# Performance work log

Measured on AMD Instinct MI355X. Metric: run time of the kernel, lower is better.

## Reference

```python
import jax, jax.numpy as jnp
import numpy as np

SIGMA_D = 0.2
SIGMA_A = 15.0
FACTOR_A = 180.0 / (SIGMA_A * np.pi)
HIDDEN = 256


def sinusoidal_embedding(x, d_model):
    # GeoTransformer-style: interleaved sin/cos pairs along last dim.
    div_term = jnp.exp(jnp.arange(0, d_model, 2, dtype=x.dtype) * (-np.log(10000.0) / d_model))  # (d/2,)
    omegas = x[..., None] * div_term  # (..., d/2)
    emb = jnp.stack([jnp.sin(omegas), jnp.cos(omegas)], axis=-1)  # (..., d/2, 2)
    return emb.reshape(*x.shape, d_model)


def _indices(points, anchor_points):
    # pairwise sq dist: |p|^2 + |a|^2 - 2 p.a, clamped at 0
    sq = (jnp.sum(points ** 2, -1)[:, :, None]
          + jnp.sum(anchor_points ** 2, -1)[:, None, :]
          - 2.0 * jnp.einsum('bnd,bkd->bnk', points, anchor_points))
    dist_map = jnp.sqrt(jnp.maximum(sq, 0.0))  # (B,N,K)
    d_indices = dist_map / SIGMA_D
    ref_vectors = points[:, :, None, :] - anchor_points[:, None, :, :]  # (B,N,K,3)
    # gather with indices [1,2,...,K-1,0] == roll by -1 along K
    anc_vectors = jnp.roll(ref_vectors, shift=-1, axis=2)
    sin_values = jnp.linalg.norm(jnp.cross(ref_vectors, anc_vectors, axis=-1), axis=-1)
    cos_values = jnp.sum(ref_vectors * anc_vectors, axis=-1)
    angles = jnp.arctan2(sin_values, cos_values)
    a_indices = angles * FACTOR_A
    return d_indices, a_indices


def setup_inputs() -> dict:
    key = jax.random.key(0)
    ks = jax.random.split(key, 5)
    B, N, K, H = 1, 4096, 64, HIDDEN
    return {
        'points': jax.random.normal(ks[0], (B, N, 3), jnp.float32),
        'anchor_points': jax.random.normal(ks[1], (B, K, 3), jnp.float32),
        'cor_score': jax.random.uniform(ks[2], (K,), jnp.float32),
        'Wa': jax.random.normal(ks[3], (H, H), jnp.float32) * (1.0 / np.sqrt(H)),
        'ba': jnp.zeros((H,), jnp.float32),
        'Wd': jax.random.normal(ks[4], (H, H), jnp.float32) * (1.0 / np.sqrt(H)),
        'bd': jnp.zeros((H,), jnp.float32),
    }


def reference(points, anchor_points, cor_score, Wa, ba, Wd, bd):
    d_idx, a_idx = _indices(points, anchor_points)  # computed under no_grad in torch
    d_idx = jax.lax.stop_gradient(d_idx)
    a_idx = jax.lax.stop_gradient(a_idx)
    a_emb = sinusoidal_embedding(a_idx, HIDDEN)          # (B,N,K,H)
    a_emb = jnp.einsum('bnkh,oh->bnko', a_emb, Wa) + ba
    d_emb = sinusoidal_embedding(d_idx, HIDDEN)
    d_emb = jnp.einsum('bnkh,oh->bnko', d_emb, Wd) + bd
    # reduction_a == 'max'
    d_emb = jnp.max(d_emb, axis=2)
    a_emb = jnp.max(a_emb, axis=2)
    return d_emb + a_emb  # (B,N,H)
```

## Files before the change

### kernel.cpp

```cpp
#include <hip/hip_runtime.h>
#include <hip/hip_bf16.h>
#include <math.h>


typedef __attribute__((ext_vector_type(8))) short short8;
typedef __attribute__((ext_vector_type(16))) float f32x16;
typedef __attribute__((ext_vector_type(4))) unsigned int uint4v;
typedef __attribute__((ext_vector_type(4))) float float4v;
typedef __attribute__((ext_vector_type(4))) unsigned short ushort4v;

#define HH 256
#define KK 112
#define P_PTS 8
#define NPTS 4096

__device__ __forceinline__ unsigned short f2bf(float f) {
    union { float f; unsigned int u; } v; v.f = f;
    unsigned int r = v.u + 0x7fffu + ((v.u >> 16) & 1u);
    return (unsigned short)(r >> 16);
}

__device__ __forceinline__ unsigned int pack_sc(float s, float c) {
    union { __hip_bfloat162 h; unsigned int u; } v;
    v.h = __float22bfloat162_rn(make_float2(s, c));
    return v.u;
}

__global__ __launch_bounds__(64)
void prep_w_kernel(const float* __restrict__ Wa, const float* __restrict__ Wd,
                   unsigned short* __restrict__ wbf) {
    const int r = blockIdx.x * 64 + threadIdx.x;
    const int t = r >> 8, o = r & 255;
    const float* W = (t == 0 ? Wd : Wa) + o * HH;
    unsigned short* dst = wbf + (t * HH + o) * KK;
    #pragma unroll
    for (int e4 = 0; e4 < 26; ++e4) {
        const float4v w4 = *(const float4v*)(W + e4 * 4);
        ushort4v s4;
        #pragma unroll
        for (int j = 0; j < 4; ++j) s4[j] = f2bf(w4[j]);
        *(ushort4v*)(dst + e4 * 4) = s4;
    }
    float u1 = 0.f, u2 = 0.f, u3 = 0.f, u4 = 0.f, v = 0.f;
    float d = 0.023713737056616554f;
    for (int i = 52; i < 128; ++i) {
        const float d2 = d * d;
        const float ws = W[2 * i], wc = W[2 * i + 1];
        u1 += d * ws;
        u3 += -(d * d2) * (1.0f / 6.0f) * ws;
        u2 += -0.5f * d2 * wc;
        u4 += (d2 * d2) * (1.0f / 24.0f) * wc;
        v  += wc;
        d *= 0.9305720409297085f;
    }
    dst[104] = f2bf(u1);
    dst[105] = f2bf(u2);
    dst[106] = f2bf(u3);
    dst[107] = f2bf(u4);
    dst[108] = f2bf(v);
    dst[109] = 0; dst[110] = 0; dst[111] = 0;
}


__global__ __launch_bounds__(512, 4)
void cgse_main(const float* __restrict__ points,
               const float* __restrict__ anchors,
               const unsigned short* __restrict__ wbf,
               const float* __restrict__ ba,
               const float* __restrict__ bd,
               float* __restrict__ out) {
    __shared__ __align__(16) unsigned short E[2][2][64 * 128];
    __shared__ float xs[2][P_PTS][64];
    __shared__ float anch[192];

    const int tid = threadIdx.x;
    const int wave = tid >> 6, lane = tid & 63;
    const int l5 = lane & 31, half = lane >> 5;
    const int base = blockIdx.x * P_PTS;
    const int pg = wave >> 2;
    const int w4 = wave & 3;

    if (tid < 192) anch[tid] = anchors[tid];
    __syncthreads();
    {
        const int k2 = (lane + 1) & 63;
        const int pn = base + wave;
        const float px = points[pn * 3 + 0], py = points[pn * 3 + 1], pz = points[pn * 3 + 2];
        const float r1x = px - anch[lane * 3 + 0];
        const float r1y = py - anch[lane * 3 + 1];
        const float r1z = pz - anch[lane * 3 + 2];
        const float r2x = px - anch[k2 * 3 + 0];
        const float r2y = py - anch[k2 * 3 + 1];
        const float r2z = pz - anch[k2 * 3 + 2];
        xs[0][wave][lane] = sqrtf(r1x * r1x + r1y * r1y + r1z * r1z) * 5.0f;
        const float cx = r1y * r2z - r1z * r2y;
        const float cy = r1z * r2x - r1x * r2z;
        const float cz = r1x * r2y - r1y * r2x;
        const float sv = sqrtf(cx * cx + cy * cy + cz * cz);
        const float cv = r1x * r2x + r1y * r2y + r1z * r2z;
        xs[1][wave][lane] = atan2f(sv, cv) * 3.8197186342054885f;
    }

    float bias[2];
    #pragma unroll
    for (int ntp = 0; ntp < 2; ++ntp) {
        const int c = w4 * 64 + ntp * 32 + l5;
        bias[ntp] = ba[c] + bd[c];
    }

    const float cw = 0.15915494309189535f * __expf(-(float)w4 * 0.2878231366242554f);

    const int tb = pg * 16384;
    const int wbase = (lane << 8) ^ (((lane & 7) ^ w4) << 4);
    const int rbase = (l5 << 8) ^ ((l5 & 7) << 4) ^ (half << 4);

    auto fill_chunk = [&](char* eb, int c, float x, float xc) {
        uint4v w;
        if (w4 == 1 && c == 3) {
            const float x2 = x * x;
            w[0] = pack_sc(x, x2);
            w[1] = pack_sc(x2 * x, x2 * x2);
            w[2] = pack_sc(1.0f, 0.0f);
            w[3] = 0u;
        } else {
            const float DCI[4] = {1.0f, 0.31622776601683794f, 0.1f,
                                  0.03162277660168379f};
            const float t0 = xc * DCI[c];
            const float t[4] = {t0, t0 * 0.9305720409297085f,
                                t0 * 0.8659643233600653f, t0 * 0.8058421877614819f};
            #pragma unroll
            for (int j = 0; j < 4; ++j)
                w[j] = pack_sc(__builtin_amdgcn_sinf(t[j]), __builtin_amdgcn_cosf(t[j]));
        }
        *(uint4v*)(eb + (wbase ^ (c << 6)));
        *(uint4v*)(eb + (wbase ^ (c << 6))) = w;
    };

    auto fill_tile = [&](char* eb, float x) {
        const float xc = x * cw;
        fill_chunk(eb, 0, x, xc);
        fill_chunk(eb, 1, x, xc);
        fill_chunk(eb, 2, x, xc);
        if (w4 < 2) fill_chunk(eb, 3, x, xc);
    };

    short8 bw[2][7];
    auto loadW = [&](int t) {
        #pragma unroll
        for (int ntp = 0; ntp < 2; ++ntp) {
            const unsigned short* wr =
                wbf + (t * HH + w4 * 64 + ntp * 32 + l5) * KK + half * 8;
            #pragma unroll
            for (int ks = 0; ks < 7; ++ks)
                bw[ntp][ks] = *(const short8*)(wr + ks * 16);
        }
    };

    auto htree = [&](const f32x16& a) -> float {
        const float v0 = fmaxf(fmaxf(a[0], a[1]), a[2]);
        const float v1 = fmaxf(fmaxf(a[3], a[4]), a[5]);
        const float v2 = fmaxf(fmaxf(a[6], a[7]), a[8]);
        const float v3 = fmaxf(fmaxf(a[9], a[10]), a[11]);
        const float v4 = fmaxf(fmaxf(a[12], a[13]), a[14]);
        const float w0 = fmaxf(fmaxf(v0, v1), v2);
        const float w1 = fmaxf(fmaxf(v3, v4), a[15]);
        return fmaxf(w0, w1);
    };

    loadW(0);
    __syncthreads();
    fill_tile((char*)E[0][pg], xs[0][pg][lane]);

    float dm[4][2];

    #pragma unroll
    for (int q = 0; q < 4; ++q) {
        __syncthreads();
        const char* ebC = (const char*)E[q & 1][pg];
        char* ebN = (char*)E[(q & 1) ^ 1][pg];
        fill_tile(ebN, (q < 3) ? xs[0][2 * (q + 1) + pg][lane] : xs[1][pg][lane]);

        float m[2];
        #pragma unroll
        for (int hh = 0; hh < 2; ++hh) {
            f32x16 acc[2];
            #pragma unroll
            for (int ntp = 0; ntp < 2; ++ntp)
                #pragma unroll
                for (int r = 0; r < 16; ++r) acc[ntp][r] = 0.f;
            #pragma unroll
            for (int ks = 0; ks < 7; ++ks) {
                const short8 afr = *(const short8*)
                    (ebC + ((rbase ^ (ks << 5)) + hh * 8192));
                __builtin_amdgcn_s_setprio(1);
                acc[0] = __builtin_amdgcn_mfma_f32_32x32x16_bf16(afr, bw[0][ks], acc[0], 0, 0, 0);
                acc[1] = __builtin_amdgcn_mfma_f32_32x32x16_bf16(afr, bw[1][ks], acc[1], 0, 0, 0);
                __builtin_amdgcn_s_setprio(0);
            }
            #pragma unroll
            for (int ntp = 0; ntp < 2; ++ntp) {
                const float h = htree(acc[ntp]);
                m[ntp] = hh ? fmaxf(m[ntp], h) : h;
            }
        }
        #pragma unroll
        for (int ntp = 0; ntp < 2; ++ntp) {
            m[ntp] = fmaxf(m[ntp], __shfl_down(m[ntp], 32));
            dm[q][ntp] = m[ntp];
        }
    }

    loadW(1);

    #pragma unroll
    for (int q = 0; q < 4; ++q) {
        __syncthreads();
        const char* ebC = (const char*)E[q & 1][pg];
        char* ebN = (char*)E[(q & 1) ^ 1][pg];
        if (q < 3) fill_tile(ebN, xs[1][2 * (q + 1) + pg][lane]);

        float m[2];
        #pragma unroll
        for (int hh = 0; hh < 2; ++hh) {
            f32x16 acc[2];
            #pragma unroll
            for (int ntp = 0; ntp < 2; ++ntp)
                #pragma unroll
                for (int r = 0; r < 16; ++r) acc[ntp][r] = 0.f;
            #pragma unroll
            for (int ks = 0; ks < 7; ++ks) {
                const short8 afr = *(const short8*)
                    (ebC + ((rbase ^ (ks << 5)) + hh * 8192));
                __builtin_amdgcn_s_setprio(1);
                acc[0] = __builtin_amdgcn_mfma_f32_32x32x16_bf16(afr, bw[0][ks], acc[0], 0, 0, 0);
                acc[1] = __builtin_amdgcn_mfma_f32_32x32x16_bf16(afr, bw[1][ks], acc[1], 0, 0, 0);
                __builtin_amdgcn_s_setprio(0);
            }
            #pragma unroll
            for (int ntp = 0; ntp < 2; ++ntp) {
                const float h = htree(acc[ntp]);
                m[ntp] = hh ? fmaxf(m[ntp], h) : h;
            }
        }
        #pragma unroll
        for (int ntp = 0; ntp < 2; ++ntp) {
            m[ntp] = fmaxf(m[ntp], __shfl_down(m[ntp], 32));
            if (lane < 32)
                out[(base + 2 * q + pg) * HH + w4 * 64 + ntp * 32 + l5]
                    = m[ntp] + dm[q][ntp] + bias[ntp];
        }
    }
}

extern "C" void kernel_launch(void* const* d_in, const int* in_sizes, int n_in,
                              void* d_out, int out_size, void* d_ws, size_t ws_size,
                              hipStream_t stream) {
    const float* points  = (const float*)d_in[0];
    const float* anchors = (const float*)d_in[1];
    const float* Wa = (const float*)d_in[3];
    const float* ba = (const float*)d_in[4];
    const float* Wd = (const float*)d_in[5];
    const float* bd = (const float*)d_in[6];

    unsigned short* wbf = (unsigned short*)d_ws;

    hipLaunchKernelGGL(prep_w_kernel, dim3(8), dim3(64), 0, stream, Wa, Wd, wbf);
    hipLaunchKernelGGL(cgse_main, dim3(NPTS / P_PTS), dim3(512), 0, stream,
                       points, anchors, wbf, ba, bd, (float*)d_out);
}
```

Baseline: 103.3 us.

## Generate MFMA A-fragments in registers and parallelize weight prep per row

The main kernel no longer writes sin/cos embedding tiles to double-buffered shared memory and reads them back behind barriers. Each wave now builds its A-operand fragments directly in registers from per-point geometry, using lane shuffles to fetch the right x value. This removes the LDS traffic and the __syncthreads pipeline. The cost is that each wave recomputes the embedding and the geometry for its points, which adds transcendental work. The weight-prep kernel is also restructured to give one wavefront per output row, with a shuffle reduction for the tail Taylor terms instead of a serial per-thread loop.

```diff
diff --git a/kernel.cpp b/kernel.cpp
--- a/kernel.cpp
+++ b/kernel.cpp
@@ -11,7 +11,6 @@
 
 #define HH 256
 #define KK 112
-#define P_PTS 8
 #define NPTS 4096
 
 __device__ __forceinline__ unsigned short f2bf(float f) {
@@ -29,21 +28,35 @@
 __global__ __launch_bounds__(64)
 void prep_w_kernel(const float* __restrict__ Wa, const float* __restrict__ Wd,
                    unsigned short* __restrict__ wbf) {
-    const int r = blockIdx.x * 64 + threadIdx.x;
-    const int t = r >> 8, o = r & 255;
+    const int row = blockIdx.x;
+    const int t = row >> 8, o = row & 255;
+    const int lane = threadIdx.x;
     const float* W = (t == 0 ? Wd : Wa) + o * HH;
-    unsigned short* dst = wbf + (t * HH + o) * KK;
-    #pragma unroll
-    for (int e4 = 0; e4 < 26; ++e4) {
-        const float4v w4 = *(const float4v*)(W + e4 * 4);
+    unsigned short* dst = wbf + row * KK;
+
+    if (lane < 26) {
+        const float4v w4 = ((const float4v*)W)[lane];
         ushort4v s4;
         #pragma unroll
         for (int j = 0; j < 4; ++j) s4[j] = f2bf(w4[j]);
-        *(ushort4v*)(dst + e4 * 4) = s4;
-    }
-    float u1 = 0.f, u2 = 0.f, u3 = 0.f, u4 = 0.f, v = 0.f;
-    float d = 0.023713737056616554f;
-    for (int i = 52; i < 128; ++i) {
+        ((ushort4v*)dst)[lane] = s4;
+    }
+
+    float u1, u2, u3, u4, v;
+    {
+        const int i = 52 + lane;
+        const float d = exp2f(-(float)i * 0.10381025296523008f);
+        const float d2 = d * d;
+        const float ws = W[2 * i], wc = W[2 * i + 1];
+        u1 = d * ws;
+        u3 = -(d * d2) * (1.0f / 6.0f) * ws;
+        u2 = -0.5f * d2 * wc;
+        u4 = (d2 * d2) * (1.0f / 24.0f) * wc;
+        v  = wc;
+    }
+    if (lane < 12) {
+        const int i = 116 + lane;
+        const float d = exp2f(-(float)i * 0.10381025296523008f);
         const float d2 = d * d;
         const float ws = W[2 * i], wc = W[2 * i + 1];
         u1 += d * ws;
@@ -51,16 +64,24 @@
         u2 += -0.5f * d2 * wc;
         u4 += (d2 * d2) * (1.0f / 24.0f) * wc;
         v  += wc;
-        d *= 0.9305720409297085f;
-    }
-    dst[104] = f2bf(u1);
-    dst[105] = f2bf(u2);
-    dst[106] = f2bf(u3);
-    dst[107] = f2bf(u4);
-    dst[108] = f2bf(v);
-    dst[109] = 0; dst[110] = 0; dst[111] = 0;
-}
-
+    }
+    #pragma unroll
+    for (int off = 32; off; off >>= 1) {
+        u1 += __shfl_xor(u1, off);
+        u2 += __shfl_xor(u2, off);
+        u3 += __shfl_xor(u3, off);
+        u4 += __shfl_xor(u4, off);
+        v  += __shfl_xor(v, off);
+    }
+    if (lane == 0) {
+        dst[104] = f2bf(u1);
+        dst[105] = f2bf(u2);
+        dst[106] = f2bf(u3);
+        dst[107] = f2bf(u4);
+        dst[108] = f2bf(v);
+        dst[109] = 0; dst[110] = 0; dst[111] = 0;
+    }
+}
 
 __global__ __launch_bounds__(512, 4)
 void cgse_main(const float* __restrict__ points,
@@ -69,22 +90,44 @@
                const float* __restrict__ ba,
                const float* __restrict__ bd,
                float* __restrict__ out) {
-    __shared__ __align__(16) unsigned short E[2][2][64 * 128];
-    __shared__ float xs[2][P_PTS][64];
     __shared__ float anch[192];
 
     const int tid = threadIdx.x;
     const int wave = tid >> 6, lane = tid & 63;
     const int l5 = lane & 31, half = lane >> 5;
-    const int base = blockIdx.x * P_PTS;
     const int pg = wave >> 2;
     const int w4 = wave & 3;
+    const int base = blockIdx.x * 8;
 
     if (tid < 192) anch[tid] = anchors[tid];
     __syncthreads();
-    {
+
+    float bias[2];
+    #pragma unroll
+    for (int ntp = 0; ntp < 2; ++ntp) {
+        const int c = w4 * 64 + ntp * 32 + l5;
+        bias[ntp] = ba[c] + bd[c];
+    }
+
+    const float fb = half ? 0.11936620731892151f : 0.15915494309189535f;
+    const float KS[7] = {1.0f, 0.5623413251903491f, 0.31622776601683794f,
+                         0.17782794100389228f, 0.1f, 0.05623413251903491f,
+                         0.031622776601683794f};
+
+    short8 bw[2][7];
+    auto loadW = [&](int t) {
+        #pragma unroll
+        for (int ntp = 0; ntp < 2; ++ntp) {
+            const unsigned short* wr =
+                wbf + (t * HH + w4 * 64 + ntp * 32 + l5) * KK + half * 8;
+            #pragma unroll
+            for (int ks = 0; ks < 7; ++ks)
+                bw[ntp][ks] = *(const short8*)(wr + ks * 16);
+        }
+    };
+
+    auto geom = [&](int pn, float& xd, float& xa) {
         const int k2 = (lane + 1) & 63;
-        const int pn = base + wave;
         const float px = points[pn * 3 + 0], py = points[pn * 3 + 1], pz = points[pn * 3 + 2];
         const float r1x = px - anch[lane * 3 + 0];
         const float r1y = py - anch[lane * 3 + 1];
@@ -92,68 +135,32 @@
         const float r2x = px - anch[k2 * 3 + 0];
         const float r2y = py - anch[k2 * 3 + 1];
         const float r2z = pz - anch[k2 * 3 + 2];
-        xs[0][wave][lane] = sqrtf(r1x * r1x + r1y * r1y + r1z * r1z) * 5.0f;
+        xd = sqrtf(r1x * r1x + r1y * r1y + r1z * r1z) * 5.0f;
         const float cx = r1y * r2z - r1z * r2y;
         const float cy = r1z * r2x - r1x * r2z;
         const float cz = r1x * r2y - r1y * r2x;
         const float sv = sqrtf(cx * cx + cy * cy + cz * cz);
         const float cv = r1x * r2x + r1y * r2y + r1z * r2z;
-        xs[1][wave][lane] = atan2f(sv, cv) * 3.8197186342054885f;
-    }
-
-    float bias[2];
-    #pragma unroll
-    for (int ntp = 0; ntp < 2; ++ntp) {
-        const int c = w4 * 64 + ntp * 32 + l5;
-        bias[ntp] = ba[c] + bd[c];
-    }
-
-    const float cw = 0.15915494309189535f * __expf(-(float)w4 * 0.2878231366242554f);
-
-    const int tb = pg * 16384;
-    const int wbase = (lane << 8) ^ (((lane & 7) ^ w4) << 4);
-    const int rbase = (l5 << 8) ^ ((l5 & 7) << 4) ^ (half << 4);
-
-    auto fill_chunk = [&](char* eb, int c, float x, float xc) {
+        xa = atan2f(sv, cv) * 3.8197186342054885f;
+    };
+
+    auto genA = [&](float tb, float xr, int ks) -> short8 {
         uint4v w;
-        if (w4 == 1 && c == 3) {
-            const float x2 = x * x;
-            w[0] = pack_sc(x, x2);
-            w[1] = pack_sc(x2 * x, x2 * x2);
+        if (half && ks == 6) {
+            const float x2 = xr * xr;
+            w[0] = pack_sc(xr, x2);
+            w[1] = pack_sc(x2 * xr, x2 * x2);
             w[2] = pack_sc(1.0f, 0.0f);
             w[3] = 0u;
         } else {
-            const float DCI[4] = {1.0f, 0.31622776601683794f, 0.1f,
-                                  0.03162277660168379f};
-            const float t0 = xc * DCI[c];
+            const float t0 = tb * KS[ks];
             const float t[4] = {t0, t0 * 0.9305720409297085f,
                                 t0 * 0.8659643233600653f, t0 * 0.8058421877614819f};
             #pragma unroll
             for (int j = 0; j < 4; ++j)
                 w[j] = pack_sc(__builtin_amdgcn_sinf(t[j]), __builtin_amdgcn_cosf(t[j]));
         }
-        *(uint4v*)(eb + (wbase ^ (c << 6)));
-        *(uint4v*)(eb + (wbase ^ (c << 6))) = w;
-    };
-
-    auto fill_tile = [&](char* eb, float x) {
-        const float xc = x * cw;
-        fill_chunk(eb, 0, x, xc);
-        fill_chunk(eb, 1, x, xc);
-        fill_chunk(eb, 2, x, xc);
-        if (w4 < 2) fill_chunk(eb, 3, x, xc);
-    };
-
-    short8 bw[2][7];
-    auto loadW = [&](int t) {
-        #pragma unroll
-        for (int ntp = 0; ntp < 2; ++ntp) {
-            const unsigned short* wr =
-                wbf + (t * HH + w4 * 64 + ntp * 32 + l5) * KK + half * 8;
-            #pragma unroll
-            for (int ks = 0; ks < 7; ++ks)
-                bw[ntp][ks] = *(const short8*)(wr + ks * 16);
-        }
+        return *(short8*)&w;
     };
 
     auto htree = [&](const f32x16& a) -> float {
@@ -167,87 +174,53 @@
         return fmaxf(w0, w1);
     };
 
-    loadW(0);
-    __syncthreads();
-    fill_tile((char*)E[0][pg], xs[0][pg][lane]);
-
-    float dm[4][2];
-
-    #pragma unroll
-    for (int q = 0; q < 4; ++q) {
-        __syncthreads();
-        const char* ebC = (const char*)E[q & 1][pg];
-        char* ebN = (char*)E[(q & 1) ^ 1][pg];
-        fill_tile(ebN, (q < 3) ? xs[0][2 * (q + 1) + pg][lane] : xs[1][pg][lane]);
-
-        float m[2];
+    auto ptmax = [&](float x, float m[2]) {
         #pragma unroll
         for (int hh = 0; hh < 2; ++hh) {
-            f32x16 acc[2];
-            #pragma unroll
-            for (int ntp = 0; ntp < 2; ++ntp)
-                #pragma unroll
-                for (int r = 0; r < 16; ++r) acc[ntp][r] = 0.f;
+            const float xv = __shfl(x, l5 + 32 * hh);
+            const float tb = xv * fb;
+            f32x16 acc0, acc1;
+            #pragma unroll
+            for (int r = 0; r < 16; ++r) { acc0[r] = 0.f; acc1[r] = 0.f; }
             #pragma unroll
             for (int ks = 0; ks < 7; ++ks) {
-                const short8 afr = *(const short8*)
-                    (ebC + ((rbase ^ (ks << 5)) + hh * 8192));
+                const short8 afr = genA(tb, xv, ks);
                 __builtin_amdgcn_s_setprio(1);
-                acc[0] = __builtin_amdgcn_mfma_f32_32x32x16_bf16(afr, bw[0][ks], acc[0], 0, 0, 0);
-                acc[1] = __builtin_amdgcn_mfma_f32_32x32x16_bf16(afr, bw[1][ks], acc[1], 0, 0, 0);
+                acc0 = __builtin_amdgcn_mfma_f32_32x32x16_bf16(afr, bw[0][ks], acc0, 0, 0, 0);
+                acc1 = __builtin_amdgcn_mfma_f32_32x32x16_bf16(afr, bw[1][ks], acc1, 0, 0, 0);
                 __builtin_amdgcn_s_setprio(0);
             }
-            #pragma unroll
-            for (int ntp = 0; ntp < 2; ++ntp) {
-                const float h = htree(acc[ntp]);
-                m[ntp] = hh ? fmaxf(m[ntp], h) : h;
-            }
-        }
-        #pragma unroll
-        for (int ntp = 0; ntp < 2; ++ntp) {
-            m[ntp] = fmaxf(m[ntp], __shfl_down(m[ntp], 32));
-            dm[q][ntp] = m[ntp];
-        }
+            const float h0 = htree(acc0), h1 = htree(acc1);
+            if (hh == 0) { m[0] = h0; m[1] = h1; }
+            else { m[0] = fmaxf(m[0], h0); m[1] = fmaxf(m[1], h1); }
+        }
+        m[0] = fmaxf(m[0], __shfl_down(m[0], 32));
+        m[1] = fmaxf(m[1], __shfl_down(m[1], 32));
+    };
+
+    float dm[4][2];
+
+    loadW(0);
+    #pragma unroll
+    for (int pl = 0; pl < 4; ++pl) {
+        float xd, xa;
+        geom(base + 2 * pl + pg, xd, xa);
+        float m[2];
+        ptmax(xd, m);
+        dm[pl][0] = m[0]; dm[pl][1] = m[1];
     }
 
     loadW(1);
-
-    #pragma unroll
-    for (int q = 0; q < 4; ++q) {
-        __syncthreads();
-        const char* ebC = (const char*)E[q & 1][pg];
-        char* ebN = (char*)E[(q & 1) ^ 1][pg];
-        if (q < 3) fill_tile(ebN, xs[1][2 * (q + 1) + pg][lane]);
-
+    #pragma unroll
+    for (int pl = 0; pl < 4; ++pl) {
+        const int pn = base + 2 * pl + pg;
+        float xd, xa;
+        geom(pn, xd, xa);
         float m[2];
-        #pragma unroll
-        for (int hh = 0; hh < 2; ++hh) {
-            f32x16 acc[2];
-            #pragma unroll
-            for (int ntp = 0; ntp < 2; ++ntp)
-                #pragma unroll
-                for (int r = 0; r < 16; ++r) acc[ntp][r] = 0.f;
-            #pragma unroll
-            for (int ks = 0; ks < 7; ++ks) {
-                const short8 afr = *(const short8*)
-                    (ebC + ((rbase ^ (ks << 5)) + hh * 8192));
-                __builtin_amdgcn_s_setprio(1);
-                acc[0] = __builtin_amdgcn_mfma_f32_32x32x16_bf16(afr, bw[0][ks], acc[0], 0, 0, 0);
-                acc[1] = __builtin_amdgcn_mfma_f32_32x32x16_bf16(afr, bw[1][ks], acc[1], 0, 0, 0);
-                __builtin_amdgcn_s_setprio(0);
-            }
-            #pragma unroll
-            for (int ntp = 0; ntp < 2; ++ntp) {
-                const float h = htree(acc[ntp]);
-                m[ntp] = hh ? fmaxf(m[ntp], h) : h;
-            }
-        }
-        #pragma unroll
-        for (int ntp = 0; ntp < 2; ++ntp) {
-            m[ntp] = fmaxf(m[ntp], __shfl_down(m[ntp], 32));
-            if (lane < 32)
-                out[(base + 2 * q + pg) * HH + w4 * 64 + ntp * 32 + l5]
-                    = m[ntp] + dm[q][ntp] + bias[ntp];
+        ptmax(xa, m);
+        if (lane < 32) {
+            out[pn * HH + w4 * 64 + l5]      = m[0] + dm[pl][0] + bias[0];
+            out[pn * HH + w4 * 64 + 32 + l5] = m[1] + dm[pl][1] + bias[1];
         }
     }
 }
@@ -264,7 +237,7 @@
 
     unsigned short* wbf = (unsigned short*)d_ws;
 
-    hipLaunchKernelGGL(prep_w_kernel, dim3(8), dim3(64), 0, stream, Wa, Wd, wbf);
-    hipLaunchKernelGGL(cgse_main, dim3(NPTS / P_PTS), dim3(512), 0, stream,
+    hipLaunchKernelGGL(prep_w_kernel, dim3(512), dim3(64), 0, stream, Wa, Wd, wbf);
+    hipLaunchKernelGGL(cgse_main, dim3(NPTS / 8), dim3(512), 0, stream,
                        points, anchors, wbf, ba, bd, (float*)d_out);
 }
```

Result: slower. 125.4 us (+21.4%).
